# Kernel optimization log

Measured on AMD Instinct MI355X. Metric: run time of the kernel, lower is better.

Reference implementation:

```python
import jax, jax.numpy as jnp
import numpy as np

SEQ_LEN = 8192
HIDDEN = 4096

def setup_inputs() -> dict:
    key = jax.random.key(0)
    k1, k2 = jax.random.split(key)
    hidden = jax.random.normal(k1, (HIDDEN,), dtype=jnp.float32)
    encoder_outputs = jax.random.normal(k2, (SEQ_LEN, 1, HIDDEN), dtype=jnp.float32)
    return {"hidden": hidden, "encoder_outputs": encoder_outputs}

def reference(hidden, encoder_outputs):
    # encoder_outputs: [S, 1, H] -> [S, H]
    enc = encoder_outputs.squeeze(1)
    # energies[i] = dot(hidden, enc[i])  (one batched GEMV instead of a per-step loop)
    energies = enc @ hidden  # [S]
    attn = jax.nn.softmax(energies, axis=0)  # [S]
    # output = enc^T @ attn  (torch.mm(enc.T, attn.unsqueeze(1)).squeeze(1))
    output = enc.T @ attn  # [H]
    return output, attn[:, None]
```

## Files before the change

### kernel.cpp

```cpp
#include <hip/hip_runtime.h>
#include <math.h>

#define S_LEN 8192
#define HDIM  4096
#define H4    (HDIM / 4)
#define P1_BLOCK 512
#define P1_WAVES 8
#define RB 8
#define SUMB 32
#define FB_ATTN 8

__device__ __forceinline__ float wave_reduce_sum(float x) {
#pragma unroll
  for (int o = 32; o > 0; o >>= 1) x += __shfl_xor(x, o, 64);
  return x;
}
__device__ __forceinline__ float wave_reduce_max(float x) {
#pragma unroll
  for (int o = 32; o > 0; o >>= 1) x = fmaxf(x, __shfl_xor(x, o, 64));
  return x;
}

__global__ __launch_bounds__(P1_BLOCK) void pass1_k(
    const float* __restrict__ enc, const float* __restrict__ hidden,
    float* __restrict__ energies, float* __restrict__ mb, float* __restrict__ lb,
    float* __restrict__ opart, int rpb) {
  const int t = threadIdx.x;
  const int b = blockIdx.x;
  const int row0 = b * rpb;
  const int row1 = min(S_LEN, row0 + rpb);

  const float4* hv = (const float4*)hidden;
  float hh[8];
  {
    const float4 h0 = hv[t];
    const float4 h1 = hv[t + P1_BLOCK];
    hh[0] = h0.x; hh[1] = h0.y; hh[2] = h0.z; hh[3] = h0.w;
    hh[4] = h1.x; hh[5] = h1.y; hh[6] = h1.z; hh[7] = h1.w;
  }

  float aa[8] = {0.f, 0.f, 0.f, 0.f, 0.f, 0.f, 0.f, 0.f};
  float m = -INFINITY, l = 0.f;

  __shared__ float red[RB * P1_WAVES];
  const int wid = t >> 6;
  const bool lane0 = (t & 63) == 0;
  const float4* encv = (const float4*)enc;

  for (int r0 = row0; r0 < row1; r0 += RB) {
    const int nr = min(RB, row1 - r0);
    float vv[RB][8];
    float d[RB];
#pragma unroll
    for (int r = 0; r < RB; ++r) {
      float4 x0 = make_float4(0.f, 0.f, 0.f, 0.f);
      float4 x1 = make_float4(0.f, 0.f, 0.f, 0.f);
      if (r < nr) {
        const float4* rp = encv + (size_t)(r0 + r) * H4;
        x0 = rp[t];
        x1 = rp[t + P1_BLOCK];
      }
      vv[r][0] = x0.x; vv[r][1] = x0.y; vv[r][2] = x0.z; vv[r][3] = x0.w;
      vv[r][4] = x1.x; vv[r][5] = x1.y; vv[r][6] = x1.z; vv[r][7] = x1.w;
    }
#pragma unroll
    for (int r = 0; r < RB; ++r) {
      float s = 0.f;
#pragma unroll
      for (int k = 0; k < 8; ++k) s = fmaf(vv[r][k], hh[k], s);
      d[r] = s;
    }
#pragma unroll
    for (int o = 32; o > 0; o >>= 1) {
#pragma unroll
      for (int r = 0; r < RB; ++r) d[r] += __shfl_xor(d[r], o, 64);
    }
    if (lane0) {
#pragma unroll
      for (int r = 0; r < RB; ++r) red[r * P1_WAVES + wid] = d[r];
    }
    __syncthreads();
    float e[RB];
#pragma unroll
    for (int r = 0; r < RB; ++r) {
      const float4 q0 = *(const float4*)&red[r * P1_WAVES];
      const float4 q1 = *(const float4*)&red[r * P1_WAVES + 4];
      e[r] = (q0.x + q0.y + q0.z + q0.w) + (q1.x + q1.y + q1.z + q1.w);
    }
    __syncthreads();
    if (t == 0) {
      for (int r = 0; r < nr; ++r) energies[r0 + r] = e[r];
    }
    float mn = m;
#pragma unroll
    for (int r = 0; r < RB; ++r)
      if (r < nr) mn = fmaxf(mn, e[r]);
    const float sc = __expf(m - mn);
    float w[RB];
    float lsum = 0.f;
#pragma unroll
    for (int r = 0; r < RB; ++r) {
      w[r] = (r < nr) ? __expf(e[r] - mn) : 0.f;
      lsum += w[r];
    }
    l = l * sc + lsum;
#pragma unroll
    for (int k = 0; k < 8; ++k) {
      float a = aa[k] * sc;
#pragma unroll
      for (int r = 0; r < RB; ++r) a = fmaf(w[r], vv[r][k], a);
      aa[k] = a;
    }
    m = mn;
  }

  float4* op = (float4*)(opart + (size_t)b * HDIM);
  op[t]            = make_float4(aa[0], aa[1], aa[2], aa[3]);
  op[t + P1_BLOCK] = make_float4(aa[4], aa[5], aa[6], aa[7]);
  if (t == 0) { mb[b] = m; lb[b] = l; }
}

__global__ __launch_bounds__(256) void finalize_k(
    const float* __restrict__ opart, const float* __restrict__ mb,
    const float* __restrict__ lb, const float* __restrict__ energies,
    float* __restrict__ out, int Gu) {
  const int t = threadIdx.x;
  const int wid = t >> 6;
  const bool lane0 = (t & 63) == 0;
  __shared__ float smax[4], ssum[4];

  float mv = -INFINITY;
  for (int g = t; g < Gu; g += 256) mv = fmaxf(mv, mb[g]);
  mv = wave_reduce_max(mv);
  if (lane0) smax[wid] = mv;
  __syncthreads();
  const float gm = fmaxf(fmaxf(smax[0], smax[1]), fmaxf(smax[2], smax[3]));

  float lv = 0.f;
  for (int g = t; g < Gu; g += 256) lv += lb[g] * __expf(mb[g] - gm);
  lv = wave_reduce_sum(lv);
  if (lane0) ssum[wid] = lv;
  __syncthreads();
  const float invL = 1.f / (ssum[0] + ssum[1] + ssum[2] + ssum[3]);

  if ((int)blockIdx.x < SUMB) {
    const int c  = blockIdx.x * 32 + (t & 31);
    const int g0 = t >> 5;
    float4 acc = {0.f, 0.f, 0.f, 0.f};
    for (int g = g0; g < Gu; g += 8) {
      const float w = __expf(mb[g] - gm) * invL;
      const float4 v = ((const float4*)opart)[(size_t)g * H4 + c];
      acc.x = fmaf(w, v.x, acc.x);
      acc.y = fmaf(w, v.y, acc.y);
      acc.z = fmaf(w, v.z, acc.z);
      acc.w = fmaf(w, v.w, acc.w);
    }
    __shared__ float4 sred[256];
    sred[t] = acc;
    __syncthreads();
    if (t < 32) {
      float4 s = sred[t];
#pragma unroll
      for (int q = 1; q < 8; ++q) {
        const float4 v = sred[q * 32 + t];
        s.x += v.x; s.y += v.y; s.z += v.z; s.w += v.w;
      }
      ((float4*)out)[blockIdx.x * 32 + t] = s;
    }
  } else {
    const int i4 = ((int)blockIdx.x - SUMB) * 256 + t;
    const float4 e = ((const float4*)energies)[i4];
    float4 a;
    a.x = __expf(e.x - gm) * invL;
    a.y = __expf(e.y - gm) * invL;
    a.z = __expf(e.z - gm) * invL;
    a.w = __expf(e.w - gm) * invL;
    ((float4*)(out + HDIM))[i4] = a;
  }
}

extern "C" void kernel_launch(void* const* d_in, const int* in_sizes, int n_in,
                              void* d_out, int out_size, void* d_ws, size_t ws_size,
                              hipStream_t stream) {
  const float* hidden = (const float*)d_in[0];
  const float* enc    = (const float*)d_in[1];
  float* out = (float*)d_out;
  float* wsf = (float*)d_ws;

  float* energies = wsf;
  float* mb       = wsf + 8192;
  float* lb       = wsf + 9216;
  float* opart    = wsf + 10240;

  const size_t avail_f = ws_size / 4;
  int Gmax = (avail_f > 10240) ? (int)((avail_f - 10240) / HDIM) : 1;
  int G = Gmax < 512 ? Gmax : 512;
  if (G < 1) G = 1;
  const int rpb = (S_LEN + G - 1) / G;
  const int Gu  = (S_LEN + rpb - 1) / rpb;

  pass1_k<<<Gu, P1_BLOCK, 0, stream>>>(enc, hidden, energies, mb, lb, opart, rpb);
  finalize_k<<<SUMB + FB_ATTN, 256, 0, stream>>>(opart, mb, lb, energies, out, Gu);
}
```

Before: 211.9 us.

## Fuse both passes into one cooperative kernel with grid-wide sync

Adds a fused kernel that computes the per-block online-softmax partials, performs a cooperative grid sync, and then does the global reduction and attention normalization in the same launch. The attention write is spread across all blocks instead of a handful. The row batch per iteration drops to 4 to fit more blocks per CU, which co-residency requires. This removes a second kernel launch and its dependency gap, but adds grid-sync cost and runtime occupancy queries on the host, and falls back to the old two-kernel path if co-residency or the workspace size is insufficient.

```diff
diff --git a/kernel.cpp b/kernel.cpp
--- a/kernel.cpp
+++ b/kernel.cpp
@@ -1,25 +1,174 @@
 #include <hip/hip_runtime.h>
+#include <hip/hip_cooperative_groups.h>
 #include <math.h>
+
+namespace cg = cooperative_groups;
 
 #define S_LEN 8192
 #define HDIM  4096
 #define H4    (HDIM / 4)
+#define BLK   512
+#define NWAVE 8
+#define RB 4
+#define GRID 512
+#define RPB  (S_LEN / GRID)
+#define SUMB 32
+#define FB_ATTN 8
+
+__device__ __forceinline__ float wave_reduce_sum(float x) {
+#pragma unroll
+  for (int o = 32; o > 0; o >>= 1) x += __shfl_xor(x, o, 64);
+  return x;
+}
+__device__ __forceinline__ float wave_reduce_max(float x) {
+#pragma unroll
+  for (int o = 32; o > 0; o >>= 1) x = fmaxf(x, __shfl_xor(x, o, 64));
+  return x;
+}
+
+__global__ __launch_bounds__(BLK, 4) void fused_k(
+    const float* __restrict__ enc, const float* __restrict__ hidden,
+    float* __restrict__ energies, float* __restrict__ mb, float* __restrict__ lb,
+    float* __restrict__ opart, float* __restrict__ out) {
+  const int t = threadIdx.x;
+  const int b = blockIdx.x;
+  const int row0 = b * RPB;
+  const int wid = t >> 6;
+  const bool lane0 = (t & 63) == 0;
+
+  __shared__ float red[RB * NWAVE];
+  __shared__ float smax[NWAVE], ssum[NWAVE];
+  __shared__ float4 sred[BLK];
+
+  const float4* hv = (const float4*)hidden;
+  float hh[8];
+  {
+    const float4 h0 = hv[t];
+    const float4 h1 = hv[t + BLK];
+    hh[0] = h0.x; hh[1] = h0.y; hh[2] = h0.z; hh[3] = h0.w;
+    hh[4] = h1.x; hh[5] = h1.y; hh[6] = h1.z; hh[7] = h1.w;
+  }
+  float aa[8] = {0.f, 0.f, 0.f, 0.f, 0.f, 0.f, 0.f, 0.f};
+  float m = -INFINITY, l = 0.f;
+  const float4* encv = (const float4*)enc;
+
+  for (int r0 = row0; r0 < row0 + RPB; r0 += RB) {
+    float vv[RB][8];
+    float d[RB];
+#pragma unroll
+    for (int r = 0; r < RB; ++r) {
+      const float4* rp = encv + (size_t)(r0 + r) * H4;
+      const float4 x0 = rp[t];
+      const float4 x1 = rp[t + BLK];
+      vv[r][0] = x0.x; vv[r][1] = x0.y; vv[r][2] = x0.z; vv[r][3] = x0.w;
+      vv[r][4] = x1.x; vv[r][5] = x1.y; vv[r][6] = x1.z; vv[r][7] = x1.w;
+    }
+#pragma unroll
+    for (int r = 0; r < RB; ++r) {
+      float s = 0.f;
+#pragma unroll
+      for (int k = 0; k < 8; ++k) s = fmaf(vv[r][k], hh[k], s);
+      d[r] = s;
+    }
+#pragma unroll
+    for (int o = 32; o > 0; o >>= 1) {
+#pragma unroll
+      for (int r = 0; r < RB; ++r) d[r] += __shfl_xor(d[r], o, 64);
+    }
+    if (lane0) {
+#pragma unroll
+      for (int r = 0; r < RB; ++r) red[r * NWAVE + wid] = d[r];
+    }
+    __syncthreads();
+    float e[RB];
+#pragma unroll
+    for (int r = 0; r < RB; ++r) {
+      const float4 q0 = *(const float4*)&red[r * NWAVE];
+      const float4 q1 = *(const float4*)&red[r * NWAVE + 4];
+      e[r] = (q0.x + q0.y + q0.z + q0.w) + (q1.x + q1.y + q1.z + q1.w);
+    }
+    __syncthreads();
+    if (t == 0) {
+#pragma unroll
+      for (int r = 0; r < RB; ++r) energies[r0 + r] = e[r];
+    }
+    float mn = m;
+#pragma unroll
+    for (int r = 0; r < RB; ++r) mn = fmaxf(mn, e[r]);
+    const float sc = __expf(m - mn);
+    float w[RB];
+    float lsum = 0.f;
+#pragma unroll
+    for (int r = 0; r < RB; ++r) { w[r] = __expf(e[r] - mn); lsum += w[r]; }
+    l = l * sc + lsum;
+#pragma unroll
+    for (int k = 0; k < 8; ++k) {
+      float a = aa[k] * sc;
+#pragma unroll
+      for (int r = 0; r < RB; ++r) a = fmaf(w[r], vv[r][k], a);
+      aa[k] = a;
+    }
+    m = mn;
+  }
+
+  {
+    float4* op = (float4*)(opart + (size_t)b * HDIM);
+    op[t]       = make_float4(aa[0], aa[1], aa[2], aa[3]);
+    op[t + BLK] = make_float4(aa[4], aa[5], aa[6], aa[7]);
+    if (t == 0) { mb[b] = m; lb[b] = l; }
+  }
+
+  cg::this_grid().sync();
+
+  const float mbt = mb[t];
+  float mv = wave_reduce_max(mbt);
+  if (lane0) smax[wid] = mv;
+  __syncthreads();
+  float gm = smax[0];
+#pragma unroll
+  for (int i = 1; i < NWAVE; ++i) gm = fmaxf(gm, smax[i]);
+
+  float lv = wave_reduce_sum(lb[t] * __expf(mbt - gm));
+  if (lane0) ssum[wid] = lv;
+  __syncthreads();
+  float L = ssum[0];
+#pragma unroll
+  for (int i = 1; i < NWAVE; ++i) L += ssum[i];
+  const float invL = 1.f / L;
+
+  if (t < RPB) {
+    out[HDIM + row0 + t] = __expf(energies[row0 + t] - gm) * invL;
+  }
+
+  if (b < SUMB) {
+    const int c  = b * SUMB + (t & 31);
+    const int g0 = t >> 5;
+    float4 acc = {0.f, 0.f, 0.f, 0.f};
+    for (int g = g0; g < GRID; g += 16) {
+      const float w = __expf(mb[g] - gm) * invL;
+      const float4 v = ((const float4*)opart)[(size_t)g * H4 + c];
+      acc.x = fmaf(w, v.x, acc.x);
+      acc.y = fmaf(w, v.y, acc.y);
+      acc.z = fmaf(w, v.z, acc.z);
+      acc.w = fmaf(w, v.w, acc.w);
+    }
+    sred[t] = acc;
+    __syncthreads();
+    if (t < 32) {
+      float4 s = sred[t];
+#pragma unroll
+      for (int q = 1; q < 16; ++q) {
+        const float4 v = sred[q * 32 + t];
+        s.x += v.x; s.y += v.y; s.z += v.z; s.w += v.w;
+      }
+      ((float4*)out)[b * SUMB + t] = s;
+    }
+  }
+}
+
 #define P1_BLOCK 512
 #define P1_WAVES 8
-#define RB 8
-#define SUMB 32
-#define FB_ATTN 8
-
-__device__ __forceinline__ float wave_reduce_sum(float x) {
-#pragma unroll
-  for (int o = 32; o > 0; o >>= 1) x += __shfl_xor(x, o, 64);
-  return x;
-}
-__device__ __forceinline__ float wave_reduce_max(float x) {
-#pragma unroll
-  for (int o = 32; o > 0; o >>= 1) x = fmaxf(x, __shfl_xor(x, o, 64));
-  return x;
-}
+#define RBF 8
 
 __global__ __launch_bounds__(P1_BLOCK) void pass1_k(
     const float* __restrict__ enc, const float* __restrict__ hidden,
@@ -38,21 +187,19 @@
     hh[0] = h0.x; hh[1] = h0.y; hh[2] = h0.z; hh[3] = h0.w;
     hh[4] = h1.x; hh[5] = h1.y; hh[6] = h1.z; hh[7] = h1.w;
   }
-
   float aa[8] = {0.f, 0.f, 0.f, 0.f, 0.f, 0.f, 0.f, 0.f};
   float m = -INFINITY, l = 0.f;
-
-  __shared__ float red[RB * P1_WAVES];
+  __shared__ float red[RBF * P1_WAVES];
   const int wid = t >> 6;
   const bool lane0 = (t & 63) == 0;
   const float4* encv = (const float4*)enc;
 
-  for (int r0 = row0; r0 < row1; r0 += RB) {
-    const int nr = min(RB, row1 - r0);
-    float vv[RB][8];
-    float d[RB];
-#pragma unroll
-    for (int r = 0; r < RB; ++r) {
+  for (int r0 = row0; r0 < row1; r0 += RBF) {
+    const int nr = min(RBF, row1 - r0);
+    float vv[RBF][8];
+    float d[RBF];
+#pragma unroll
+    for (int r = 0; r < RBF; ++r) {
       float4 x0 = make_float4(0.f, 0.f, 0.f, 0.f);
       float4 x1 = make_float4(0.f, 0.f, 0.f, 0.f);
       if (r < nr) {
@@ -64,7 +211,7 @@
       vv[r][4] = x1.x; vv[r][5] = x1.y; vv[r][6] = x1.z; vv[r][7] = x1.w;
     }
 #pragma unroll
-    for (int r = 0; r < RB; ++r) {
+    for (int r = 0; r < RBF; ++r) {
       float s = 0.f;
 #pragma unroll
       for (int k = 0; k < 8; ++k) s = fmaf(vv[r][k], hh[k], s);
@@ -73,16 +220,16 @@
 #pragma unroll
     for (int o = 32; o > 0; o >>= 1) {
 #pragma unroll
-      for (int r = 0; r < RB; ++r) d[r] += __shfl_xor(d[r], o, 64);
+      for (int r = 0; r < RBF; ++r) d[r] += __shfl_xor(d[r], o, 64);
     }
     if (lane0) {
 #pragma unroll
-      for (int r = 0; r < RB; ++r) red[r * P1_WAVES + wid] = d[r];
-    }
-    __syncthreads();
-    float e[RB];
-#pragma unroll
-    for (int r = 0; r < RB; ++r) {
+      for (int r = 0; r < RBF; ++r) red[r * P1_WAVES + wid] = d[r];
+    }
+    __syncthreads();
+    float e[RBF];
+#pragma unroll
+    for (int r = 0; r < RBF; ++r) {
       const float4 q0 = *(const float4*)&red[r * P1_WAVES];
       const float4 q1 = *(const float4*)&red[r * P1_WAVES + 4];
       e[r] = (q0.x + q0.y + q0.z + q0.w) + (q1.x + q1.y + q1.z + q1.w);
@@ -93,13 +240,13 @@
     }
     float mn = m;
 #pragma unroll
-    for (int r = 0; r < RB; ++r)
+    for (int r = 0; r < RBF; ++r)
       if (r < nr) mn = fmaxf(mn, e[r]);
     const float sc = __expf(m - mn);
-    float w[RB];
+    float w[RBF];
     float lsum = 0.f;
 #pragma unroll
-    for (int r = 0; r < RB; ++r) {
+    for (int r = 0; r < RBF; ++r) {
       w[r] = (r < nr) ? __expf(e[r] - mn) : 0.f;
       lsum += w[r];
     }
@@ -108,7 +255,7 @@
     for (int k = 0; k < 8; ++k) {
       float a = aa[k] * sc;
 #pragma unroll
-      for (int r = 0; r < RB; ++r) a = fmaf(w[r], vv[r][k], a);
+      for (int r = 0; r < RBF; ++r) a = fmaf(w[r], vv[r][k], a);
       aa[k] = a;
     }
     m = mn;
@@ -194,11 +341,30 @@
 
   const size_t avail_f = ws_size / 4;
   int Gmax = (avail_f > 10240) ? (int)((avail_f - 10240) / HDIM) : 1;
-  int G = Gmax < 512 ? Gmax : 512;
+  int G = Gmax < GRID ? Gmax : GRID;
   if (G < 1) G = 1;
   const int rpb = (S_LEN + G - 1) / G;
   const int Gu  = (S_LEN + rpb - 1) / rpb;
 
+  bool coop = (Gu == GRID && rpb == RPB);
+  if (coop) {
+    int nb = 0;
+    if (hipOccupancyMaxActiveBlocksPerMultiprocessor(
+            &nb, (const void*)fused_k, BLK, 0) != hipSuccess) nb = 0;
+    int dev = 0, cus = 0;
+    hipGetDevice(&dev);
+    hipDeviceGetAttribute(&cus, hipDeviceAttributeMultiprocessorCount, dev);
+    if ((long)nb * cus < GRID) coop = false;
+  }
+
+  if (coop) {
+    void* args[] = {(void*)&enc, (void*)&hidden, (void*)&energies,
+                    (void*)&mb, (void*)&lb, (void*)&opart, (void*)&out};
+    if (hipLaunchCooperativeKernel((const void*)fused_k, dim3(GRID), dim3(BLK),
+                                   args, 0, stream) == hipSuccess)
+      return;
+  }
+
   pass1_k<<<Gu, P1_BLOCK, 0, stream>>>(enc, hidden, energies, mb, lb, opart, rpb);
   finalize_k<<<SUMB + FB_ATTN, 256, 0, stream>>>(opart, mb, lb, energies, out, Gu);
 }
```

After: 211.9 us. About the same (+0.0%).

## Assign rows to single waves to drop block-level syncs in fused attention

Applied to the files above, without the earlier changes.

The first pass now lets each 64-lane wave own 8 full rows, with 16 float4 per lane. The energy dot product reduces within the wave only, so the per-row-group __syncthreads and LDS reduction go away, and the online softmax keeps its state per wave. The cost is 1024 partial output vectors (16 MB) instead of 512, which finalize must read back. Finalize is reshaped to 128 column blocks with precomputed weights in shared memory. The larger register footprint (64 acc plus 64 loaded values per lane) may reduce occupancy, and the row loads arrive serially per wave.

```diff
diff --git a/kernel.cpp b/kernel.cpp
--- a/kernel.cpp
+++ b/kernel.cpp
@@ -3,11 +3,13 @@
 
 #define S_LEN 8192
 #define HDIM  4096
-#define H4    (HDIM / 4)
-#define P1_BLOCK 512
-#define P1_WAVES 8
-#define RB 8
-#define SUMB 32
+#define H4    1024
+#define ABLK  256
+#define AGRID 256
+#define AWPB  4
+#define NWAVES (AGRID * AWPB)
+#define RPW   (S_LEN / NWAVES)
+#define CBLK  128
 #define FB_ATTN 8
 
 __device__ __forceinline__ float wave_reduce_sum(float x) {
@@ -21,134 +23,108 @@
   return x;
 }
 
-__global__ __launch_bounds__(P1_BLOCK) void pass1_k(
+__global__ __launch_bounds__(ABLK) void wavegemv_k(
     const float* __restrict__ enc, const float* __restrict__ hidden,
-    float* __restrict__ energies, float* __restrict__ mb, float* __restrict__ lb,
-    float* __restrict__ opart, int rpb) {
+    float* __restrict__ energies, float* __restrict__ mw, float* __restrict__ lw,
+    float* __restrict__ opart) {
   const int t = threadIdx.x;
-  const int b = blockIdx.x;
-  const int row0 = b * rpb;
-  const int row1 = min(S_LEN, row0 + rpb);
+  const int lane = t & 63;
+  const int wid = t >> 6;
 
-  const float4* hv = (const float4*)hidden;
-  float hh[8];
+  __shared__ float4 hs[H4];
   {
-    const float4 h0 = hv[t];
-    const float4 h1 = hv[t + P1_BLOCK];
-    hh[0] = h0.x; hh[1] = h0.y; hh[2] = h0.z; hh[3] = h0.w;
-    hh[4] = h1.x; hh[5] = h1.y; hh[6] = h1.z; hh[7] = h1.w;
+    const float4* hv = (const float4*)hidden;
+#pragma unroll
+    for (int k = 0; k < 4; ++k) hs[t + k * ABLK] = hv[t + k * ABLK];
+  }
+  __syncthreads();
+
+  const int gw = blockIdx.x * AWPB + wid;
+  const int r0 = gw * RPW;
+
+  float4 acc[16];
+#pragma unroll
+  for (int k = 0; k < 16; ++k) acc[k] = make_float4(0.f, 0.f, 0.f, 0.f);
+  float m = -INFINITY, l = 0.f;
+
+  const float4* encv = (const float4*)enc;
+  for (int r = r0; r < r0 + RPW; ++r) {
+    const float4* rp = encv + (size_t)r * H4 + lane;
+    float4 v[16];
+#pragma unroll
+    for (int k = 0; k < 16; ++k) v[k] = rp[k * 64];
+    float d = 0.f;
+#pragma unroll
+    for (int k = 0; k < 16; ++k) {
+      const float4 h = hs[lane + k * 64];
+      d = fmaf(v[k].x, h.x, d);
+      d = fmaf(v[k].y, h.y, d);
+      d = fmaf(v[k].z, h.z, d);
+      d = fmaf(v[k].w, h.w, d);
+    }
+    d = wave_reduce_sum(d);
+    if (lane == 0) energies[r] = d;
+    if (d > m) {
+      const float sc = __expf(m - d);
+      l *= sc;
+#pragma unroll
+      for (int k = 0; k < 16; ++k) {
+        acc[k].x *= sc; acc[k].y *= sc; acc[k].z *= sc; acc[k].w *= sc;
+      }
+      m = d;
+    }
+    const float w = __expf(d - m);
+    l += w;
+#pragma unroll
+    for (int k = 0; k < 16; ++k) {
+      acc[k].x = fmaf(w, v[k].x, acc[k].x);
+      acc[k].y = fmaf(w, v[k].y, acc[k].y);
+      acc[k].z = fmaf(w, v[k].z, acc[k].z);
+      acc[k].w = fmaf(w, v[k].w, acc[k].w);
+    }
   }
 
-  float aa[8] = {0.f, 0.f, 0.f, 0.f, 0.f, 0.f, 0.f, 0.f};
-  float m = -INFINITY, l = 0.f;
-
-  __shared__ float red[RB * P1_WAVES];
-  const int wid = t >> 6;
-  const bool lane0 = (t & 63) == 0;
-  const float4* encv = (const float4*)enc;
-
-  for (int r0 = row0; r0 < row1; r0 += RB) {
-    const int nr = min(RB, row1 - r0);
-    float vv[RB][8];
-    float d[RB];
+  float4* op = (float4*)(opart + (size_t)gw * HDIM);
 #pragma unroll
-    for (int r = 0; r < RB; ++r) {
-      float4 x0 = make_float4(0.f, 0.f, 0.f, 0.f);
-      float4 x1 = make_float4(0.f, 0.f, 0.f, 0.f);
-      if (r < nr) {
-        const float4* rp = encv + (size_t)(r0 + r) * H4;
-        x0 = rp[t];
-        x1 = rp[t + P1_BLOCK];
-      }
-      vv[r][0] = x0.x; vv[r][1] = x0.y; vv[r][2] = x0.z; vv[r][3] = x0.w;
-      vv[r][4] = x1.x; vv[r][5] = x1.y; vv[r][6] = x1.z; vv[r][7] = x1.w;
-    }
-#pragma unroll
-    for (int r = 0; r < RB; ++r) {
-      float s = 0.f;
-#pragma unroll
-      for (int k = 0; k < 8; ++k) s = fmaf(vv[r][k], hh[k], s);
-      d[r] = s;
-    }
-#pragma unroll
-    for (int o = 32; o > 0; o >>= 1) {
-#pragma unroll
-      for (int r = 0; r < RB; ++r) d[r] += __shfl_xor(d[r], o, 64);
-    }
-    if (lane0) {
-#pragma unroll
-      for (int r = 0; r < RB; ++r) red[r * P1_WAVES + wid] = d[r];
-    }
-    __syncthreads();
-    float e[RB];
-#pragma unroll
-    for (int r = 0; r < RB; ++r) {
-      const float4 q0 = *(const float4*)&red[r * P1_WAVES];
-      const float4 q1 = *(const float4*)&red[r * P1_WAVES + 4];
-      e[r] = (q0.x + q0.y + q0.z + q0.w) + (q1.x + q1.y + q1.z + q1.w);
-    }
-    __syncthreads();
-    if (t == 0) {
-      for (int r = 0; r < nr; ++r) energies[r0 + r] = e[r];
-    }
-    float mn = m;
-#pragma unroll
-    for (int r = 0; r < RB; ++r)
-      if (r < nr) mn = fmaxf(mn, e[r]);
-    const float sc = __expf(m - mn);
-    float w[RB];
-    float lsum = 0.f;
-#pragma unroll
-    for (int r = 0; r < RB; ++r) {
-      w[r] = (r < nr) ? __expf(e[r] - mn) : 0.f;
-      lsum += w[r];
-    }
-    l = l * sc + lsum;
-#pragma unroll
-    for (int k = 0; k < 8; ++k) {
-      float a = aa[k] * sc;
-#pragma unroll
-      for (int r = 0; r < RB; ++r) a = fmaf(w[r], vv[r][k], a);
-      aa[k] = a;
-    }
-    m = mn;
-  }
-
-  float4* op = (float4*)(opart + (size_t)b * HDIM);
-  op[t]            = make_float4(aa[0], aa[1], aa[2], aa[3]);
-  op[t + P1_BLOCK] = make_float4(aa[4], aa[5], aa[6], aa[7]);
-  if (t == 0) { mb[b] = m; lb[b] = l; }
+  for (int k = 0; k < 16; ++k) op[lane + k * 64] = acc[k];
+  if (lane == 0) { mw[gw] = m; lw[gw] = l; }
 }
 
 __global__ __launch_bounds__(256) void finalize_k(
-    const float* __restrict__ opart, const float* __restrict__ mb,
-    const float* __restrict__ lb, const float* __restrict__ energies,
-    float* __restrict__ out, int Gu) {
+    const float* __restrict__ opart, const float* __restrict__ mw,
+    const float* __restrict__ lw, const float* __restrict__ energies,
+    float* __restrict__ out) {
   const int t = threadIdx.x;
+  const int b = blockIdx.x;
   const int wid = t >> 6;
   const bool lane0 = (t & 63) == 0;
+
+  __shared__ float wg[NWAVES];
   __shared__ float smax[4], ssum[4];
 
   float mv = -INFINITY;
-  for (int g = t; g < Gu; g += 256) mv = fmaxf(mv, mb[g]);
+  for (int g = t; g < NWAVES; g += 256) mv = fmaxf(mv, mw[g]);
   mv = wave_reduce_max(mv);
   if (lane0) smax[wid] = mv;
   __syncthreads();
   const float gm = fmaxf(fmaxf(smax[0], smax[1]), fmaxf(smax[2], smax[3]));
 
   float lv = 0.f;
-  for (int g = t; g < Gu; g += 256) lv += lb[g] * __expf(mb[g] - gm);
+  for (int g = t; g < NWAVES; g += 256) lv += lw[g] * __expf(mw[g] - gm);
   lv = wave_reduce_sum(lv);
   if (lane0) ssum[wid] = lv;
   __syncthreads();
   const float invL = 1.f / (ssum[0] + ssum[1] + ssum[2] + ssum[3]);
 
-  if ((int)blockIdx.x < SUMB) {
-    const int c  = blockIdx.x * 32 + (t & 31);
-    const int g0 = t >> 5;
+  for (int g = t; g < NWAVES; g += 256) wg[g] = __expf(mw[g] - gm) * invL;
+  __syncthreads();
+
+  if (b < CBLK) {
+    const int c  = b * 8 + (t & 7);
+    const int g0 = t >> 3;
     float4 acc = {0.f, 0.f, 0.f, 0.f};
-    for (int g = g0; g < Gu; g += 8) {
-      const float w = __expf(mb[g] - gm) * invL;
+    for (int g = g0; g < NWAVES; g += 32) {
+      const float w = wg[g];
       const float4 v = ((const float4*)opart)[(size_t)g * H4 + c];
       acc.x = fmaf(w, v.x, acc.x);
       acc.y = fmaf(w, v.y, acc.y);
@@ -158,17 +134,17 @@
     __shared__ float4 sred[256];
     sred[t] = acc;
     __syncthreads();
-    if (t < 32) {
+    if (t < 8) {
       float4 s = sred[t];
 #pragma unroll
-      for (int q = 1; q < 8; ++q) {
-        const float4 v = sred[q * 32 + t];
+      for (int q = 1; q < 32; ++q) {
+        const float4 v = sred[q * 8 + t];
         s.x += v.x; s.y += v.y; s.z += v.z; s.w += v.w;
       }
-      ((float4*)out)[blockIdx.x * 32 + t] = s;
+      ((float4*)out)[b * 8 + t] = s;
     }
   } else {
-    const int i4 = ((int)blockIdx.x - SUMB) * 256 + t;
+    const int i4 = (b - CBLK) * 256 + t;
     const float4 e = ((const float4*)energies)[i4];
     float4 a;
     a.x = __expf(e.x - gm) * invL;
@@ -188,17 +164,10 @@
   float* wsf = (float*)d_ws;
 
   float* energies = wsf;
-  float* mb       = wsf + 8192;
-  float* lb       = wsf + 9216;
-  float* opart    = wsf + 10240;
+  float* mw       = wsf + 8192;
+  float* lw       = wsf + 8192 + 1024;
+  float* opart    = wsf + 8192 + 2048;
 
-  const size_t avail_f = ws_size / 4;
-  int Gmax = (avail_f > 10240) ? (int)((avail_f - 10240) / HDIM) : 1;
-  int G = Gmax < 512 ? Gmax : 512;
-  if (G < 1) G = 1;
-  const int rpb = (S_LEN + G - 1) / G;
-  const int Gu  = (S_LEN + rpb - 1) / rpb;
-
-  pass1_k<<<Gu, P1_BLOCK, 0, stream>>>(enc, hidden, energies, mb, lb, opart, rpb);
-  finalize_k<<<SUMB + FB_ATTN, 256, 0, stream>>>(opart, mb, lb, energies, out, Gu);
+  wavegemv_k<<<AGRID, ABLK, 0, stream>>>(enc, hidden, energies, mw, lw, opart);
+  finalize_k<<<CBLK + FB_ATTN, 256, 0, stream>>>(opart, mw, lw, energies, out);
 }
```

After: 209.5 us. About the same (-1.1%).
